# Kernel tuning notes

Hardware: AMD Instinct MI355X
Metric: run time of the kernel (lower is better)

## Reference

```python
import jax, jax.numpy as jnp
import numpy as np

NUM_EMB = 1024
EMB_DIM = 64
COMMIT = 0.25


def setup_inputs() -> dict:
    key = jax.random.key(0)
    k1, k2 = jax.random.split(key)
    z = jax.random.normal(k1, (32, EMB_DIM, 64, 64), dtype=jnp.float32)  # [B, C, H, W]
    emb_weight = jax.random.uniform(k2, (NUM_EMB, EMB_DIM), dtype=jnp.float32,
                                    minval=-1.0 / NUM_EMB, maxval=1.0 / NUM_EMB)
    return {"z": z, "emb_weight": emb_weight}


def reference(z, emb_weight):
    B, C, H, W = z.shape  # C == embedding_dim
    # channel-last flatten: [B*H*W, C]
    z_flat = jnp.transpose(z, (0, 2, 3, 1)).reshape(-1, C)
    # ||z||^2 - 2 z.E^T + ||E||^2 -> [N, num_embeddings]
    distances = (jnp.sum(z_flat * z_flat, axis=1, keepdims=True)
                 - 2.0 * (z_flat @ emb_weight.T)
                 + jnp.sum(emb_weight * emb_weight, axis=1))
    encoding_indices = jnp.argmin(distances, axis=1)  # [N]
    # NOTE: faithful to torch's .view(z.shape) (no permute back) — layout bug preserved
    quantized = emb_weight[encoding_indices].reshape(z.shape)
    encoding_loss = jnp.mean((jax.lax.stop_gradient(z) - quantized) ** 2)
    commitment_loss = jnp.mean((z - jax.lax.stop_gradient(quantized)) ** 2)
    loss = encoding_loss + COMMIT * commitment_loss
    # straight-through estimator
    quantized = z + jax.lax.stop_gradient(quantized - z)
    return quantized, loss, encoding_indices.reshape(B, H, W)
```

## Files before the change

### kernel.cpp

```cpp
#include <hip/hip_runtime.h>
#include <hip/hip_bf16.h>

#define NPOS  131072
#define NEMB  1024
#define DIM   64
#define NELEM 8388608
#define HW    4096

#define EMBF32_OFF 0
#define EE_OFF     65536
#define EE24_OFF   66560
#define EHI_OFF    67584
#define IDX_OFF    133120
#define CNT_OFF    264192
#define FLAG_OFF   264193
#define CNT2_OFF   264194
#define CNT3_OFF   264195
#define PART_OFF   264196
#define WL_OFF     268292
#define WLP_OFF    301060
#define WL2_OFF    333828
#define ZT_OFF     344064
#define CAPP       32768
#define CAPF       8192
#define W24L       671
#define W24F       4194
#define WRSF       1400.0f
#define WRSL       671.0f
#define KSCALE     16777216.0f
#define NEG2S      -33554432.0f
#define KCLAMP     2080374.0f
#define PAIRW      7168
#define FULLB      256
#define LCAPP      256
#define LCAPF      64

typedef short bf16x8 __attribute__((ext_vector_type(8)));
typedef float f32x4  __attribute__((ext_vector_type(4)));
typedef unsigned short u16x4 __attribute__((ext_vector_type(4)));

__device__ __forceinline__ float b2f(unsigned short u) {
  return __uint_as_float((unsigned)u << 16);
}
__device__ __forceinline__ unsigned short f2b_rne(float f) {
  unsigned u = __float_as_uint(f);
  unsigned r = u + 0x7FFF + ((u >> 16) & 1);
  return (unsigned short)(r >> 16);
}
__device__ __forceinline__ int med3i(int a, int b, int c) {
  int d;
  asm("v_med3_i32 %0, %1, %2, %3" : "=v"(d) : "v"(a), "v"(b), "v"(c));
  return d;
}
__device__ __forceinline__ void kins4(int& K1, int& K2, int& K3, int& K4, int key) {
  int nk1 = min(K1, key);
  int nk2 = med3i(K1, K2, key);
  int nk3 = med3i(K2, K3, key);
  int nk4 = med3i(K3, K4, key);
  K1 = nk1; K2 = nk2; K3 = nk3; K4 = nk4;
}

__global__ __launch_bounds__(256) void k0_prep(const unsigned int* __restrict__ z,
                                               const void* __restrict__ emb,
                                               float* __restrict__ ws,
                                               int zt_ok) {
  __shared__ int sflag;
  __shared__ float tile[64 * 65];
  int tid = threadIdx.x;
  if (tid < 64) {
    unsigned short vz = ((const unsigned short*)z)[2 * tid];
    int ez = (vz >> 7) & 0xFF;
    unsigned long long mz = __ballot(ez >= 121 && ez <= 131);
    unsigned short ve = ((const unsigned short*)emb)[2 * tid];
    int eex = (ve >> 7) & 0xFF;
    unsigned long long me = __ballot(eex >= 96 && eex <= 118);
    int f = 0;
    if (__popcll(mz) >= 32) f |= 1;
    if (__popcll(me) >= 32) f |= 2;
    if (tid == 0) sflag = f;
    if (blockIdx.x == 0) {
      unsigned eu = ((const unsigned*)emb)[tid * 500];
      unsigned long long mel = __ballot((eu & 0xFFFFu) == 0);
      unsigned zu = z[tid * 65536];
      unsigned long long mzl = __ballot((zu & 0xFFFFu) == 0);
      if (tid == 0) {
        int F = f;
        if (mzl == ~0ull) F |= 4;
        if (mel == ~0ull) F |= 8;
        ((int*)ws)[FLAG_OFF] = F;
        ((int*)ws)[CNT_OFF] = 0;
        ((int*)ws)[CNT2_OFF] = 0;
        ((int*)ws)[CNT3_OFF] = 0;
      }
    }
  }
  __syncthreads();
  int flagz = sflag & 1, flage = sflag & 2;

  if (blockIdx.x < 256) {
    unsigned short* EHI = (unsigned short*)(ws + EHI_OFF);
    int wv = tid >> 6, lane = tid & 63;
    int e = blockIdx.x * 4 + wv;
    float v;
    unsigned short hi;
    if (flage) {
      hi = ((const unsigned short*)emb)[e * DIM + lane];
      v = b2f(hi);
    } else {
      v = ((const float*)emb)[e * DIM + lane];
      hi = f2b_rne(v);
    }
    ws[EMBF32_OFF + e * DIM + lane] = v;
    EHI[e * DIM + lane] = hi;
    float sq = __fmul_rn(v, v);
    float r[8];
#pragma unroll
    for (int q = 0; q < 8; ++q) r[q] = __shfl(sq, q, 64);
#pragma unroll
    for (int t = 1; t < 8; ++t)
#pragma unroll
      for (int q = 0; q < 8; ++q)
        r[q] = __fadd_rn(r[q], __shfl(sq, t * 8 + q, 64));
    float lft = __fadd_rn(__fadd_rn(r[0], r[1]), __fadd_rn(r[2], r[3]));
    float rgt = __fadd_rn(__fadd_rn(r[4], r[5]), __fadd_rn(r[6], r[7]));
    float eev = __fadd_rn(lft, rgt);
    if (lane == 0) {
      ws[EE_OFF + e] = eev;
      ws[EE24_OFF + e] = __fmul_rn(eev, KSCALE);
    }
  }

  if (zt_ok) {
    float* zT = ws + ZT_OFF;
    int b = blockIdx.x >> 6, hw0 = (blockIdx.x & 63) * 64;
    if (flagz) {
      const unsigned short* zs_ = (const unsigned short*)z;
      for (int i = tid; i < 4096; i += 256) {
        int c = i >> 6, x = i & 63;
        tile[c * 65 + x] = b2f(zs_[(size_t)b * 262144 + (size_t)c * 4096 + hw0 + x]);
      }
    } else {
      const float* zf = (const float*)z;
      for (int i = tid; i < 4096; i += 256) {
        int c = i >> 6, x = i & 63;
        tile[c * 65 + x] = zf[(size_t)b * 262144 + (size_t)c * 4096 + hw0 + x];
      }
    }
    __syncthreads();
    for (int i = tid; i < 4096; i += 256) {
      int nl = i >> 6, c = i & 63;
      zT[((size_t)b * 4096 + hw0 + nl) * 64 + c] = tile[c * 65 + nl];
    }
  }
}

__global__ __launch_bounds__(1024, 1) void k1(const void* __restrict__ zv,
                                              const float* __restrict__ ws,
                                              int* __restrict__ idx,
                                              int* __restrict__ cnt,
                                              int* __restrict__ cnt2,
                                              int* __restrict__ wl,
                                              int* __restrict__ wlp,
                                              int* __restrict__ wl2) {
  int flag = ((const int*)ws)[FLAG_OFF];
  bool zbf = flag & 5, ebf = flag & 10;
  int wth = (zbf && ebf) ? W24L : W24F;
  float wrs = (zbf && ebf) ? WRSL : WRSF;
  bool zlo_live = !(flag & 1);
  __shared__ uint4 sE[8192];
  __shared__ f32x4 see24v[256];
  __shared__ int lc[2];
  __shared__ int lbase[2];
  __shared__ int lpos[LCAPP];
  __shared__ int lpk[LCAPP];
  __shared__ int lposF[LCAPF];
  int tid = threadIdx.x;
  if (tid < 2) lc[tid] = 0;
  const uint4* EHIg = (const uint4*)(ws + EHI_OFF);
  for (int i = tid; i < 8192; i += 1024) {
    int row = i >> 3, c = i & 7;
    sE[row * 8 + (c ^ (row & 7))] = EHIg[i];
  }
  {
    float* ps = (float*)see24v;
    if (tid < 1024) ps[tid] = ws[EE24_OFF + tid];
  }
  __syncthreads();

  int wv = tid >> 6, lane = tid & 63;
  int mcol = lane & 15, g = lane >> 4;
  int posb = blockIdx.x * 512 + wv * 32;
  int b = posb >> 12;
  int col0 = (posb & 4095) + mcol;

  bf16x8 Z[2][2], Zlo[2][2];
  if (flag & 1) {
    const unsigned short* zb = (const unsigned short*)zv + (size_t)b * 262144;
#pragma unroll
    for (int s = 0; s < 2; ++s)
#pragma unroll
      for (int j = 0; j < 8; ++j) {
        size_t ro = (size_t)(s * 32 + g * 8 + j) * 4096;
#pragma unroll
        for (int t = 0; t < 2; ++t)
          Z[t][s][j] = (short)zb[ro + col0 + t * 16];
      }
  } else {
    const float* zb = (const float*)zv + (size_t)b * 262144;
#pragma unroll
    for (int s = 0; s < 2; ++s)
#pragma unroll
      for (int j = 0; j < 8; ++j) {
        size_t ro = (size_t)(s * 32 + g * 8 + j) * 4096;
#pragma unroll
        for (int t = 0; t < 2; ++t) {
          float v = zb[ro + col0 + t * 16];
          unsigned short h = f2b_rne(v);
          Z[t][s][j] = (short)h;
          Zlo[t][s][j] = (short)f2b_rne(__fsub_rn(v, b2f(h)));
        }
      }
  }

  int K1a[2], K2a[2], K3a[2], K4a[2];
#pragma unroll
  for (int t = 0; t < 2; ++t) {
    K1a[t] = 0x7FFFFFFF; K2a[t] = 0x7FFFFFFF; K3a[t] = 0x7FFFFFFF; K4a[t] = 0x7FFFFFFF;
  }
  const f32x4 zero = {0.f, 0.f, 0.f, 0.f};
  int sw = mcol & 7;
  int slot0 = g ^ sw, slot1 = (4 + g) ^ sw;

  __builtin_amdgcn_s_setprio(1);
#pragma unroll 4
  for (int nt = 0; nt < 64; ++nt) {
    int erow = nt * 16 + mcol;
    bf16x8 h0 = *(const bf16x8*)&sE[erow * 8 + slot0];
    bf16x8 h1 = *(const bf16x8*)&sE[erow * 8 + slot1];
    int cbase = nt * 16 + g * 4;
    f32x4 ee4 = see24v[nt * 4 + g];
#pragma unroll
    for (int t = 0; t < 2; ++t) {
      f32x4 acc = __builtin_amdgcn_mfma_f32_16x16x32_bf16(h0, Z[t][0], zero, 0, 0, 0);
      acc = __builtin_amdgcn_mfma_f32_16x16x32_bf16(h1, Z[t][1], acc, 0, 0, 0);
#pragma unroll
      for (int r = 0; r < 4; ++r) {
        float xf = __builtin_fmaf(acc[r], NEG2S, ee4[r]);
        xf = __builtin_amdgcn_fmed3f(xf, -KCLAMP, KCLAMP);
        kins4(K1a[t], K2a[t], K3a[t], K4a[t], ((int)xf << 10) | (cbase + r));
      }
    }
  }
  __builtin_amdgcn_s_setprio(0);
#pragma unroll
  for (int d = 16; d < 64; d <<= 1) {
#pragma unroll
    for (int t = 0; t < 2; ++t) {
      int o1 = __shfl_xor(K1a[t], d, 64);
      int o2 = __shfl_xor(K2a[t], d, 64);
      int o3 = __shfl_xor(K3a[t], d, 64);
      int o4 = __shfl_xor(K4a[t], d, 64);
      kins4(K1a[t], K2a[t], K3a[t], K4a[t], o1);
      kins4(K1a[t], K2a[t], K3a[t], K4a[t], o2);
      kins4(K1a[t], K2a[t], K3a[t], K4a[t], o3);
      kins4(K1a[t], K2a[t], K3a[t], K4a[t], o4);
    }
  }
  float CA[2], CB[2], CC[2];
#pragma unroll
  for (int t = 0; t < 2; ++t) {
    int v1 = K1a[t] >> 10, v2 = K2a[t] >> 10, v3 = K3a[t] >> 10;
    float c1 = (float)v1, c2 = (float)v2, c3 = 1e30f;
    bool need = (v2 - v1 < wth);
    bool has3 = (v3 - v1 < wth);
    if (need) {
      if (zlo_live) {
        int i1 = K1a[t] & 1023, i2 = K2a[t] & 1023, i3 = K3a[t] & 1023;
        bf16x8 e10 = *(const bf16x8*)&sE[i1 * 8 + (g ^ (i1 & 7))];
        bf16x8 e11 = *(const bf16x8*)&sE[i1 * 8 + ((4 + g) ^ (i1 & 7))];
        bf16x8 e20 = *(const bf16x8*)&sE[i2 * 8 + (g ^ (i2 & 7))];
        bf16x8 e21 = *(const bf16x8*)&sE[i2 * 8 + ((4 + g) ^ (i2 & 7))];
        bf16x8 e30 = e10, e31 = e11;
        if (has3) {
          e30 = *(const bf16x8*)&sE[i3 * 8 + (g ^ (i3 & 7))];
          e31 = *(const bf16x8*)&sE[i3 * 8 + ((4 + g) ^ (i3 & 7))];
        }
        float cr1 = 0.f, cr2 = 0.f, cr3 = 0.f;
#pragma unroll
        for (int j = 0; j < 8; ++j) {
          float zl0 = b2f((unsigned short)Zlo[t][0][j]);
          float zl1 = b2f((unsigned short)Zlo[t][1][j]);
          cr1 = __builtin_fmaf(zl0, b2f((unsigned short)e10[j]), cr1);
          cr1 = __builtin_fmaf(zl1, b2f((unsigned short)e11[j]), cr1);
          cr2 = __builtin_fmaf(zl0, b2f((unsigned short)e20[j]), cr2);
          cr2 = __builtin_fmaf(zl1, b2f((unsigned short)e21[j]), cr2);
          cr3 = __builtin_fmaf(zl0, b2f((unsigned short)e30[j]), cr3);
          cr3 = __builtin_fmaf(zl1, b2f((unsigned short)e31[j]), cr3);
        }
        cr1 += __shfl_xor(cr1, 16, 64); cr2 += __shfl_xor(cr2, 16, 64); cr3 += __shfl_xor(cr3, 16, 64);
        cr1 += __shfl_xor(cr1, 32, 64); cr2 += __shfl_xor(cr2, 32, 64); cr3 += __shfl_xor(cr3, 32, 64);
        c1 = __builtin_fmaf(cr1, NEG2S, c1);
        c2 = __builtin_fmaf(cr2, NEG2S, c2);
        if (has3) c3 = __builtin_fmaf(cr3, NEG2S, (float)v3);
      } else {
        if (has3) c3 = (float)v3;
      }
    }
    CA[t] = c1; CB[t] = c2; CC[t] = c3;
  }
  if (lane < 16) {
#pragma unroll
    for (int t = 0; t < 2; ++t) {
      int npos = posb + t * 16 + mcol;
      int i1 = K1a[t] & 1023;
      int v1 = K1a[t] >> 10, v2 = K2a[t] >> 10, v4 = K4a[t] >> 10;
      if (v2 - v1 >= wth) {
        idx[npos] = i1;
      } else {
        float cA = CA[t], cB = CB[t], cC = CC[t];
        int iA = i1, iB = K2a[t] & 1023, iC = K3a[t] & 1023;
        if (cB < cA || (cB == cA && iB < iA)) { float tf = cA; cA = cB; cB = tf; int ti = iA; iA = iB; iB = ti; }
        if (cC < cB || (cC == cB && iC < iB)) { float tf = cB; cB = cC; cC = tf; int ti = iB; iB = iC; iC = ti; }
        if (cB < cA || (cB == cA && iB < iA)) { float tf = cA; cA = cB; cB = tf; int ti = iA; iA = iB; iB = ti; }
        idx[npos] = iA;
        if (v4 - v1 < wth) {
          int sf = atomicAdd(&lc[1], 1);
          if (sf < LCAPF) { lposF[sf] = npos; }
          else { int s2 = atomicAdd(cnt2, 1); if (s2 < CAPF) wl2[s2] = npos; }
        } else if (cB - cA < wrs) {
          if (cC - cA < wrs) {
            int sf = atomicAdd(&lc[1], 1);
            if (sf < LCAPF) { lposF[sf] = npos; }
            else { int s2 = atomicAdd(cnt2, 1); if (s2 < CAPF) wl2[s2] = npos; }
          } else {
            int pk = (iA << 10) | iB;
            int sl = atomicAdd(&lc[0], 1);
            if (sl < LCAPP) { lpos[sl] = npos; lpk[sl] = pk; }
            else { int s2 = atomicAdd(cnt, 1); if (s2 < CAPP) { wl[s2] = npos; wlp[s2] = pk; } }
          }
        }
      }
    }
  }
  __syncthreads();
  if (tid == 0 && lc[0] > 0) lbase[0] = atomicAdd(cnt, min(lc[0], LCAPP));
  if (tid == 1 && lc[1] > 0) lbase[1] = atomicAdd(cnt2, min(lc[1], LCAPF));
  __syncthreads();
  int npl = min(lc[0], LCAPP);
  for (int i = tid; i < npl; i += 1024) {
    int d = lbase[0] + i;
    if (d < CAPP) { wl[d] = lpos[i]; wlp[d] = lpk[i]; }
  }
  int nfl = min(lc[1], LCAPF);
  for (int i = tid; i < nfl; i += 1024) {
    int d = lbase[1] + i;
    if (d < CAPF) wl2[d] = lposF[i];
  }
}

__global__ __launch_bounds__(256) void k2(const void* __restrict__ zv,
                                          const float* __restrict__ ws,
                                          const int* __restrict__ cntp,
                                          const int* __restrict__ wl,
                                          const int* __restrict__ wlp,
                                          const int* __restrict__ cntf,
                                          const int* __restrict__ wl2,
                                          int* __restrict__ idx,
                                          int zt_ok) {
  int flag_z = ((const int*)ws)[FLAG_OFF] & 1;
  const float* Ef = ws + EMBF32_OFF;
  const float* ee = ws + EE_OFF;
  const float* zT = ws + ZT_OFF;
  if (blockIdx.x < 1792) {
    int mcnt = *cntp;
    if (mcnt > CAPP) mcnt = CAPP;
    int lane = threadIdx.x & 63;
    int gw = (blockIdx.x * 256 + threadIdx.x) >> 6;
    for (int j = gw; j < mcnt; j += PAIRW) {
      int n = wl[j];
      int pk = wlp[j];
      int ia = (pk >> 10) & 1023, ib = pk & 1023;
      float zk;
      if (zt_ok) {
        zk = zT[(size_t)n * 64 + lane];
      } else {
        int b = n >> 12, hw = n & 4095;
        size_t off = (size_t)b * 262144 + (size_t)lane * 4096 + hw;
        zk = flag_z ? b2f(((const unsigned short*)zv)[off])
                    : ((const float*)zv)[off];
      }
      float sq = __fmul_rn(zk, zk);
      float r[8];
#pragma unroll
      for (int q = 0; q < 8; ++q) r[q] = __shfl(sq, q, 64);
#pragma unroll
      for (int t = 1; t < 8; ++t)
#pragma unroll
        for (int q = 0; q < 8; ++q)
          r[q] = __fadd_rn(r[q], __shfl(sq, t * 8 + q, 64));
      float lft = __fadd_rn(__fadd_rn(r[0], r[1]), __fadd_rn(r[2], r[3]));
      float rgt = __fadd_rn(__fadd_rn(r[4], r[5]), __fadd_rn(r[6], r[7]));
      float t1 = __fadd_rn(lft, rgt);
      double pa = (double)Ef[ia * DIM + lane] * (double)zk;
      double pb = (double)Ef[ib * DIM + lane] * (double)zk;
#pragma unroll
      for (int d = 32; d > 0; d >>= 1) {
        pa += __shfl_xor(pa, d, 64);
        pb += __shfl_xor(pb, d, 64);
      }
      float da = __fadd_rn(__fsub_rn(t1, __fmul_rn(2.0f, (float)pa)), ee[ia]);
      float db = __fadd_rn(__fsub_rn(t1, __fmul_rn(2.0f, (float)pb)), ee[ib]);
      int win = (db < da) ? ib : ((da < db) ? ia : (ia < ib ? ia : ib));
      if (lane == 0) idx[n] = win;
    }
  } else {
    __shared__ float zs[DIM];
    __shared__ float t1s;
    __shared__ float bval[256];
    __shared__ int bidx[256];
    int m = *cntf;
    if (m > CAPF) m = CAPF;
    int tid = threadIdx.x;
    for (int j = (int)blockIdx.x - 1792; j < m; j += FULLB) {
      int n = wl2[j];
      __syncthreads();
      if (tid < 64) {
        float zk;
        if (zt_ok) {
          zk = zT[(size_t)n * 64 + tid];
        } else {
          int b = n >> 12, hw = n & 4095;
          size_t off = (size_t)b * 262144 + (size_t)tid * 4096 + hw;
          zk = flag_z ? b2f(((const unsigned short*)zv)[off])
                      : ((const float*)zv)[off];
        }
        zs[tid] = zk;
        float sq = __fmul_rn(zk, zk);
        float r[8];
#pragma unroll
        for (int q = 0; q < 8; ++q) r[q] = __shfl(sq, q, 64);
#pragma unroll
        for (int t = 1; t < 8; ++t)
#pragma unroll
          for (int q = 0; q < 8; ++q)
            r[q] = __fadd_rn(r[q], __shfl(sq, t * 8 + q, 64));
        float lft = __fadd_rn(__fadd_rn(r[0], r[1]), __fadd_rn(r[2], r[3]));
        float rgt = __fadd_rn(__fadd_rn(r[4], r[5]), __fadd_rn(r[6], r[7]));
        if (tid == 0) t1s = __fadd_rn(lft, rgt);
      }
      __syncthreads();
      float t1 = t1s;
      float best = 1e30f;
      int bi = 0;
      int e0 = tid * 4;
      for (int e = e0; e < e0 + 4; ++e) {
        const float* E0 = Ef + e * DIM;
        double a = 0.0;
#pragma unroll 1
        for (int k = 0; k < DIM; ++k)
          a = fma((double)E0[k], (double)zs[k], a);
        float ahat = (float)a;
        float d = __fadd_rn(__fsub_rn(t1, __fmul_rn(2.0f, ahat)), ee[e]);
        if (d < best) { best = d; bi = e; }
      }
      bval[tid] = best;
      bidx[tid] = bi;
      __syncthreads();
      for (int s = 128; s > 0; s >>= 1) {
        if (tid < s) {
          float vb = bval[tid + s];
          int ibx = bidx[tid + s];
          if (vb < bval[tid] || (vb == bval[tid] && ibx < bidx[tid])) {
            bval[tid] = vb;
            bidx[tid] = ibx;
          }
        }
        __syncthreads();
      }
      if (tid == 0) idx[n] = bidx[0];
    }
  }
}

__global__ __launch_bounds__(256) void k3_out(const void* __restrict__ zv,
                                              const float* __restrict__ ws,
                                              const int* __restrict__ idx,
                                              float* __restrict__ out,
                                              double* __restrict__ part) {
  int flag_z = ((const int*)ws)[FLAG_OFF] & 1;
  const float* Ef = ws + EMBF32_OFF;
  int g = blockIdx.x * 256 + threadIdx.x;
  if (g < NPOS)
    out[(size_t)NELEM + 1 + (size_t)g] = (float)idx[g];
  int base = g >> 4, c = (g & 15) * 4;
  int e4[4];
#pragma unroll
  for (int i = 0; i < 4; ++i) e4[i] = idx[base + i * 32768];
  f32x4 q[4];
#pragma unroll
  for (int i = 0; i < 4; ++i) q[i] = *(const f32x4*)&Ef[e4[i] * DIM + c];
  f32x4 zV[4];
  if (flag_z) {
    const unsigned short* zp = (const unsigned short*)zv;
#pragma unroll
    for (int i = 0; i < 4; ++i) {
      int m = (g + i * 524288) * 4;
      u16x4 zu = __builtin_nontemporal_load((const u16x4*)(zp + m));
      zV[i][0] = b2f(zu[0]); zV[i][1] = b2f(zu[1]);
      zV[i][2] = b2f(zu[2]); zV[i][3] = b2f(zu[3]);
    }
  } else {
    const float* zp = (const float*)zv;
#pragma unroll
    for (int i = 0; i < 4; ++i) {
      int m = (g + i * 524288) * 4;
      zV[i] = __builtin_nontemporal_load((const f32x4*)(zp + m));
    }
  }
  float acc = 0.f;
#pragma unroll
  for (int i = 0; i < 4; ++i) {
    int m = (g + i * 524288) * 4;
    __builtin_nontemporal_store(q[i], (f32x4*)&out[m]);
#pragma unroll
    for (int r = 0; r < 4; ++r) {
      float d = zV[i][r] - q[i][r];
      acc = __builtin_fmaf(d, d, acc);
    }
  }
  for (int off = 32; off > 0; off >>= 1) acc += __shfl_down(acc, off);
  __shared__ float ps[4];
  if ((threadIdx.x & 63) == 0) ps[threadIdx.x >> 6] = acc;
  __syncthreads();
  if (threadIdx.x == 0) part[blockIdx.x] = (double)(ps[0] + ps[1] + ps[2] + ps[3]);
}

__global__ __launch_bounds__(256) void k4_final(const double* __restrict__ part,
                                                float* __restrict__ out) {
  __shared__ double sh[256];
  double a = 0.0;
#pragma unroll
  for (int j = 0; j < 8; ++j) a += part[threadIdx.x + j * 256];
  sh[threadIdx.x] = a;
  __syncthreads();
  for (int s = 128; s > 0; s >>= 1) {
    if ((int)threadIdx.x < s) sh[threadIdx.x] += sh[threadIdx.x + s];
    __syncthreads();
  }
  if (threadIdx.x == 0)
    out[NELEM] = (float)(1.25 * sh[0] / (double)NELEM);
}

extern "C" void kernel_launch(void* const* d_in, const int* in_sizes, int n_in,
                              void* d_out, int out_size, void* d_ws, size_t ws_size,
                              hipStream_t stream) {
  const void* z   = d_in[0];
  const void* emb = d_in[1];
  float* out = (float*)d_out;
  float* ws = (float*)d_ws;
  int* wsI = (int*)d_ws;
  int* idx  = wsI + IDX_OFF;
  int* cnt  = wsI + CNT_OFF;
  int* cnt2 = wsI + CNT2_OFF;
  int* wl   = wsI + WL_OFF;
  int* wlp  = wsI + WLP_OFF;
  int* wl2  = wsI + WL2_OFF;
  double* part = (double*)(ws + PART_OFF);
  int zt_ok = (ws_size >= (size_t)(ZT_OFF + NELEM) * 4) ? 1 : 0;

  hipLaunchKernelGGL(k0_prep, dim3(2048), dim3(256), 0, stream,
                     (const unsigned int*)z, emb, ws, zt_ok);
  hipLaunchKernelGGL(k1, dim3(256), dim3(1024), 0, stream,
                     z, ws, idx, cnt, cnt2, wl, wlp, wl2);
  hipLaunchKernelGGL(k2, dim3(2048), dim3(256), 0, stream,
                     z, ws, cnt, wl, wlp, cnt2, wl2, idx, zt_ok);
  hipLaunchKernelGGL(k3_out, dim3(2048), dim3(256), 0, stream,
                     z, ws, idx, out, part);
  hipLaunchKernelGGL(k4_final, dim3(1), dim3(256), 0, stream, part, out);
}
```

Before: 216.9 us.

## Route ambiguous triples to cheap 3-candidate rescoring instead of full search

Near-tie positions whose top three approximate candidates are all close are now rescored exactly on those three candidates in the pair worklist, rather than sent to the full 1024-entry fallback. The packed candidate word grows from two indices to three, the pair worklist capacity is enlarged, and block counts are rebalanced between the pair and full-search paths. The full-search dot product is unrolled into four independent double accumulators to shorten the dependency chain. This cuts expensive full rescoring work, but assumes the true argmin is among the top three whenever the fourth candidate is outside the margin. The reordered double summation can also change rounding slightly.

```diff
diff --git a/kernel.cpp b/kernel.cpp
--- a/kernel.cpp
+++ b/kernel.cpp
@@ -18,10 +18,10 @@
 #define CNT3_OFF   264195
 #define PART_OFF   264196
 #define WL_OFF     268292
-#define WLP_OFF    301060
-#define WL2_OFF    333828
-#define ZT_OFF     344064
-#define CAPP       32768
+#define WLP_OFF    317444
+#define WL2_OFF    366596
+#define ZT_OFF     376832
+#define CAPP       49152
 #define CAPF       8192
 #define W24L       671
 #define W24F       4194
@@ -30,8 +30,8 @@
 #define KSCALE     16777216.0f
 #define NEG2S      -33554432.0f
 #define KCLAMP     2080374.0f
-#define PAIRW      7168
-#define FULLB      256
+#define PAIRW      6144
+#define FULLB      512
 #define LCAPP      256
 #define LCAPF      64
 
@@ -316,6 +316,11 @@
       int v1 = K1a[t] >> 10, v2 = K2a[t] >> 10, v4 = K4a[t] >> 10;
       if (v2 - v1 >= wth) {
         idx[npos] = i1;
+      } else if (v4 - v1 < wth) {
+        idx[npos] = i1;
+        int sf = atomicAdd(&lc[1], 1);
+        if (sf < LCAPF) { lposF[sf] = npos; }
+        else { int s2 = atomicAdd(cnt2, 1); if (s2 < CAPF) wl2[s2] = npos; }
       } else {
         float cA = CA[t], cB = CB[t], cC = CC[t];
         int iA = i1, iB = K2a[t] & 1023, iC = K3a[t] & 1023;
@@ -323,21 +328,11 @@
         if (cC < cB || (cC == cB && iC < iB)) { float tf = cB; cB = cC; cC = tf; int ti = iB; iB = iC; iC = ti; }
         if (cB < cA || (cB == cA && iB < iA)) { float tf = cA; cA = cB; cB = tf; int ti = iA; iA = iB; iB = ti; }
         idx[npos] = iA;
-        if (v4 - v1 < wth) {
-          int sf = atomicAdd(&lc[1], 1);
-          if (sf < LCAPF) { lposF[sf] = npos; }
-          else { int s2 = atomicAdd(cnt2, 1); if (s2 < CAPF) wl2[s2] = npos; }
-        } else if (cB - cA < wrs) {
-          if (cC - cA < wrs) {
-            int sf = atomicAdd(&lc[1], 1);
-            if (sf < LCAPF) { lposF[sf] = npos; }
-            else { int s2 = atomicAdd(cnt2, 1); if (s2 < CAPF) wl2[s2] = npos; }
-          } else {
-            int pk = (iA << 10) | iB;
-            int sl = atomicAdd(&lc[0], 1);
-            if (sl < LCAPP) { lpos[sl] = npos; lpk[sl] = pk; }
-            else { int s2 = atomicAdd(cnt, 1); if (s2 < CAPP) { wl[s2] = npos; wlp[s2] = pk; } }
-          }
+        if (cB - cA < wrs) {
+          int pk = (iA << 20) | (iB << 10) | iC;
+          int sl = atomicAdd(&lc[0], 1);
+          if (sl < LCAPP) { lpos[sl] = npos; lpk[sl] = pk; }
+          else { int s2 = atomicAdd(cnt, 1); if (s2 < CAPP) { wl[s2] = npos; wlp[s2] = pk; } }
         }
       }
     }
@@ -371,7 +366,7 @@
   const float* Ef = ws + EMBF32_OFF;
   const float* ee = ws + EE_OFF;
   const float* zT = ws + ZT_OFF;
-  if (blockIdx.x < 1792) {
+  if (blockIdx.x < 1536) {
     int mcnt = *cntp;
     if (mcnt > CAPP) mcnt = CAPP;
     int lane = threadIdx.x & 63;
@@ -379,7 +374,7 @@
     for (int j = gw; j < mcnt; j += PAIRW) {
       int n = wl[j];
       int pk = wlp[j];
-      int ia = (pk >> 10) & 1023, ib = pk & 1023;
+      int ia = pk >> 20, ib = (pk >> 10) & 1023, ic = pk & 1023;
       float zk;
       if (zt_ok) {
         zk = zT[(size_t)n * 64 + lane];
@@ -403,14 +398,20 @@
       float t1 = __fadd_rn(lft, rgt);
       double pa = (double)Ef[ia * DIM + lane] * (double)zk;
       double pb = (double)Ef[ib * DIM + lane] * (double)zk;
+      double pc = (double)Ef[ic * DIM + lane] * (double)zk;
 #pragma unroll
       for (int d = 32; d > 0; d >>= 1) {
         pa += __shfl_xor(pa, d, 64);
         pb += __shfl_xor(pb, d, 64);
+        pc += __shfl_xor(pc, d, 64);
       }
       float da = __fadd_rn(__fsub_rn(t1, __fmul_rn(2.0f, (float)pa)), ee[ia]);
       float db = __fadd_rn(__fsub_rn(t1, __fmul_rn(2.0f, (float)pb)), ee[ib]);
-      int win = (db < da) ? ib : ((da < db) ? ia : (ia < ib ? ia : ib));
+      float dc = __fadd_rn(__fsub_rn(t1, __fmul_rn(2.0f, (float)pc)), ee[ic]);
+      int win = ia;
+      float dw = da;
+      if (db < dw || (db == dw && ib < win)) { win = ib; dw = db; }
+      if (dc < dw || (dc == dw && ic < win)) { win = ic; }
       if (lane == 0) idx[n] = win;
     }
   } else {
@@ -421,7 +422,7 @@
     int m = *cntf;
     if (m > CAPF) m = CAPF;
     int tid = threadIdx.x;
-    for (int j = (int)blockIdx.x - 1792; j < m; j += FULLB) {
+    for (int j = (int)blockIdx.x - 1536; j < m; j += FULLB) {
       int n = wl2[j];
       __syncthreads();
       if (tid < 64) {
@@ -455,11 +456,15 @@
       int e0 = tid * 4;
       for (int e = e0; e < e0 + 4; ++e) {
         const float* E0 = Ef + e * DIM;
-        double a = 0.0;
-#pragma unroll 1
-        for (int k = 0; k < DIM; ++k)
-          a = fma((double)E0[k], (double)zs[k], a);
-        float ahat = (float)a;
+        double a0 = 0.0, a1 = 0.0, a2 = 0.0, a3 = 0.0;
+#pragma unroll
+        for (int k = 0; k < DIM; k += 4) {
+          a0 = fma((double)E0[k],     (double)zs[k],     a0);
+          a1 = fma((double)E0[k + 1], (double)zs[k + 1], a1);
+          a2 = fma((double)E0[k + 2], (double)zs[k + 2], a2);
+          a3 = fma((double)E0[k + 3], (double)zs[k + 3], a3);
+        }
+        float ahat = (float)((a0 + a1) + (a2 + a3));
         float d = __fadd_rn(__fsub_rn(t1, __fmul_rn(2.0f, ahat)), ee[e]);
         if (d < best) { best = d; bi = e; }
       }
```

After: 174.2 us. 1.24x faster.
